# Kernel optimization log

Hardware: AMD Instinct MI355X
Metric: run time of the kernel (lower is better)

The kernel has to match this reference:

```python
import jax, jax.numpy as jnp
import numpy as np

B, L, D, H = 2, 8192, 1024, 16
HD = D // H  # head_dim = 64


def setup_inputs() -> dict:
    key = jax.random.key(0)
    ks = jax.random.split(key, 5)
    s = 1.0 / np.sqrt(D)
    return {
        "x": jax.random.normal(ks[0], (B, L, D), dtype=jnp.float32),
        "Wq": jax.random.normal(ks[1], (D, D), dtype=jnp.float32) * s,
        "bq": jnp.zeros((D,), dtype=jnp.float32),
        "Wk": jax.random.normal(ks[2], (D, D), dtype=jnp.float32) * s,
        "bk": jnp.zeros((D,), dtype=jnp.float32),
        "Wv": jax.random.normal(ks[3], (D, D), dtype=jnp.float32) * s,
        "bv": jnp.zeros((D,), dtype=jnp.float32),
        "Wo": jax.random.normal(ks[4], (D, D), dtype=jnp.float32) * s,
        "bo": jnp.zeros((D,), dtype=jnp.float32),
    }


def _rotary(seq_len, dim):
    pos = jnp.arange(seq_len, dtype=jnp.float32)
    freq = 1.0 / (10000.0 ** (jnp.arange(0, dim, 2, dtype=jnp.float32) / dim))
    ang = pos[:, None] * freq[None, :]               # (L, dim/2)
    sin, cos = jnp.sin(ang), jnp.cos(ang)
    # interleave-duplicate: stack((s,s),-1).reshape(L,dim)  (matches torch code)
    sin = jnp.stack((sin, sin), axis=-1).reshape(seq_len, dim)
    cos = jnp.stack((cos, cos), axis=-1).reshape(seq_len, dim)
    return sin, cos


def _rotate_half(t):
    t1, t2 = jnp.split(t, 2, axis=-1)
    return jnp.concatenate([-t2, t1], axis=-1)


def reference(x, Wq, bq, Wk, bk, Wv, bv, Wo, bo):
    b, l, d = x.shape
    q = (x @ Wq + bq).reshape(b, l, H, HD)
    k = (x @ Wk + bk).reshape(b, l, H, HD)
    v = (x @ Wv + bv).reshape(b, l, H, HD)

    sin, cos = _rotary(l, HD)
    sin = sin[None, :, None, :]  # (1, L, 1, HD)
    cos = cos[None, :, None, :]
    q = q * cos + _rotate_half(q) * sin
    k = k * cos + _rotate_half(k) * sin

    # NOTE: faithful to original — heads NOT transposed to (B,H,L,HD),
    # so scores are (B, L, H, H): attention mixes across heads per position.
    scores = jnp.einsum('blhd,bled->blhe', q, k) / jnp.sqrt(jnp.float32(HD))
    w = jax.nn.softmax(scores, axis=-1)              # dropout = identity (eval)
    out = jnp.einsum('blhe,bled->blhd', w, v).reshape(b, l, d)
    return out @ Wo + bo
```

## Files before the change

kernel.cpp:

```cpp
#include <hip/hip_runtime.h>
#include <hip/hip_bf16.h>

typedef __bf16 bf16_t;
typedef __bf16 bf16x8 __attribute__((ext_vector_type(8)));
typedef float f32x4 __attribute__((ext_vector_type(4)));

#define SEQ_L 8192
#define DMODEL 1024
#define NHEAD 16
#define HDIM 64
static constexpr int MROWS = 2 * SEQ_L;

__device__ __forceinline__ void async_cp16(const bf16_t* g, bf16_t* l) {
  __builtin_amdgcn_global_load_lds(
      (__attribute__((address_space(1))) void*)(void*)(g),
      (__attribute__((address_space(3))) void*)(void*)(l), 16, 0, 0);
}
__device__ __forceinline__ void wg_barrier() { __builtin_amdgcn_s_barrier(); }

__global__ __launch_bounds__(256) void f32_to_bf16_k(const float* __restrict__ in,
                                                     bf16_t* __restrict__ out, int n) {
  int i = (blockIdx.x * 256 + threadIdx.x) * 8;
  if (i >= n) return;
  float4 a = *(const float4*)(in + i);
  float4 b = *(const float4*)(in + i + 4);
  bf16x8 o;
  o[0] = (__bf16)a.x; o[1] = (__bf16)a.y; o[2] = (__bf16)a.z; o[3] = (__bf16)a.w;
  o[4] = (__bf16)b.x; o[5] = (__bf16)b.y; o[6] = (__bf16)b.z; o[7] = (__bf16)b.w;
  *(bf16x8*)(out + i) = o;
}

__global__ __launch_bounds__(256) void w_to_bt_k(
    const float* __restrict__ W0, const float* __restrict__ W1,
    const float* __restrict__ W2, const float* __restrict__ W3,
    bf16_t* __restrict__ T0, bf16_t* __restrict__ T1,
    bf16_t* __restrict__ T2, bf16_t* __restrict__ T3) {
  __shared__ float tile[32][33];
  const int z = blockIdx.z;
  const float* W = (z == 0) ? W0 : (z == 1) ? W1 : (z == 2) ? W2 : W3;
  bf16_t* T = (z == 0) ? T0 : (z == 1) ? T1 : (z == 2) ? T2 : T3;
  const int bx = blockIdx.x, by = blockIdx.y;
  const int tx = threadIdx.x, ty = threadIdx.y;
#pragma unroll
  for (int r = 0; r < 4; ++r)
    tile[ty + r * 8][tx] = W[(size_t)(by * 32 + ty + r * 8) * DMODEL + bx * 32 + tx];
  __syncthreads();
#pragma unroll
  for (int r = 0; r < 4; ++r)
    T[(size_t)(bx * 32 + ty + r * 8) * DMODEL + by * 32 + tx] = (bf16_t)tile[tx][ty + r * 8];
}

__global__ __launch_bounds__(256) void rope_tab_k(float2* __restrict__ tab) {
  int i = blockIdx.x * 256 + threadIdx.x;
  int pos = i >> 5, j = i & 31;
  double freq = pow(10000.0, -(double)j / 32.0);
  double ang = (double)pos * freq;
  tab[i] = make_float2((float)cos(ang), (float)sin(ang));
}

template <int MODE>
__global__ __launch_bounds__(256, 4) void gemm128(
    const bf16_t* __restrict__ A, const bf16_t* __restrict__ Bt,
    const float* __restrict__ b0, const float* __restrict__ b1,
    const float* __restrict__ b2, const float2* __restrict__ rope,
    void* __restrict__ O0, void* __restrict__ O1, void* __restrict__ O2) {
  constexpr int K = DMODEL;
  constexpr int NS = K / 32;
  __shared__ bf16_t As_[2][128 * 32];
  __shared__ bf16_t Bs_[2][128 * 32];
  const int tid = threadIdx.x;
  const int lane = tid & 63;
  const int wave = tid >> 6;
  const int wm = wave >> 1;
  const int wn = wave & 1;
  const size_t row0 = (size_t)blockIdx.x * 128;
  const int col0 = blockIdx.y * 128;
  const int fr = lane & 15;
  const int fke = (lane >> 4) * 8;

  const bf16_t* gA = A + (row0 + (tid >> 2)) * K + (tid & 3) * 8;
  const bf16_t* gB = Bt + ((size_t)col0 + (tid >> 2)) * K + (tid & 3) * 8;

#define STAGE(j, buf)                                      \
  do {                                                     \
    async_cp16(gA + (j)*32, &As_[buf][tid * 8]);           \
    async_cp16(gA + 64 * K + (j)*32, &As_[buf][2048 + tid * 8]); \
    async_cp16(gB + (j)*32, &Bs_[buf][tid * 8]);           \
    async_cp16(gB + 64 * K + (j)*32, &Bs_[buf][2048 + tid * 8]); \
  } while (0)
#define RD(base, row) (*(const bf16x8*)((base) + (row)*32 + fke))
#define VMCNT(n) asm volatile("s_waitcnt vmcnt(" #n ")")
#define SCHED_FENCE() __builtin_amdgcn_sched_barrier(0)

  f32x4 acc[4][4] = {};
  bf16x8 a4[4], b4[4];

#define KSTEP(CUR, DO_STAGE, JNEXT)                                            \
  do {                                                                         \
    if (DO_STAGE) STAGE(JNEXT, (CUR) ^ 1);                                     \
    _Pragma("unroll") for (int f = 0; f < 4; ++f)                              \
        a4[f] = RD(As_[CUR], wm * 64 + f * 16 + fr);                           \
    _Pragma("unroll") for (int n = 0; n < 4; ++n)                              \
        b4[n] = RD(Bs_[CUR], wn * 64 + n * 16 + fr);                           \
    __builtin_amdgcn_s_setprio(1);                                             \
    _Pragma("unroll") for (int f = 0; f < 4; ++f)                              \
        _Pragma("unroll") for (int n = 0; n < 4; ++n)                          \
            acc[f][n] = __builtin_amdgcn_mfma_f32_16x16x32_bf16(               \
                a4[f], b4[n], acc[f][n], 0, 0, 0);                             \
    __builtin_amdgcn_s_setprio(0);                                             \
    VMCNT(0);                                                                  \
    wg_barrier();                                                              \
    SCHED_FENCE();                                                             \
  } while (0)

  STAGE(0, 0);
  VMCNT(0);
  wg_barrier();
  SCHED_FENCE();

#pragma unroll 1
  for (int mm = 0; mm < NS / 2; ++mm) {
    const int m0 = 2 * mm;
    KSTEP(0, true, m0 + 1);
    KSTEP(1, (mm < NS / 2 - 1), m0 + 2);
  }
#undef KSTEP
#undef STAGE
#undef RD
#undef VMCNT
#undef SCHED_FENCE

  const int lr = (lane >> 4) * 4;
  const int lc = lane & 15;
  const int gcol = col0 + wn * 64;
  int which = 0;
  const float* bias = b0;
  int ocol = gcol;
  if constexpr (MODE == 0) {
    which = gcol >> 10;
    bias = (which == 0) ? b0 : (which == 1) ? b1 : b2;
    ocol = gcol - (which << 10);
  }
  const bool do_rope = (MODE == 0) && (which < 2);
  bf16_t* Cb = nullptr;
  float* Cf = nullptr;
  if constexpr (MODE == 0)
    Cb = (bf16_t*)((which == 0) ? O0 : (which == 1) ? O1 : O2);
  else
    Cf = (float*)O0;

#pragma unroll
  for (int mf = 0; mf < 4; ++mf) {
#pragma unroll
    for (int i = 0; i < 4; ++i) {
      const size_t grow = row0 + wm * 64 + mf * 16 + lr + i;
      float vv[4];
#pragma unroll
      for (int n = 0; n < 4; ++n) vv[n] = acc[mf][n][i] + bias[ocol + n * 16 + lc];
      if (do_rope) {
        const int pos = (int)(grow & (size_t)(SEQ_L - 1));
        const float2* rp = rope + (size_t)pos * 32 + (lc >> 1);
        float rv[4];
#pragma unroll
        for (int n = 0; n < 4; ++n) {
          float2 cs = rp[n * 8];
          rv[n] = (n < 2) ? vv[n] * cs.x - vv[n + 2] * cs.y
                          : vv[n] * cs.x + vv[n - 2] * cs.y;
        }
#pragma unroll
        for (int n = 0; n < 4; ++n) vv[n] = rv[n];
      }
      const size_t cbase = grow * (size_t)DMODEL + ocol + lc;
      if constexpr (MODE == 1) {
#pragma unroll
        for (int n = 0; n < 4; ++n) Cf[cbase + n * 16] = vv[n];
      } else {
#pragma unroll
        for (int n = 0; n < 4; ++n) Cb[cbase + n * 16] = (bf16_t)vv[n];
      }
    }
  }
}

__global__ __launch_bounds__(256) void attn_heads_k(const bf16_t* __restrict__ qb,
                                                    const bf16_t* __restrict__ kb,
                                                    const bf16_t* __restrict__ vb,
                                                    bf16_t* __restrict__ ob) {
  const int t = blockIdx.x * 256 + threadIdx.x;
  const int row = t >> 4;
  const int h = t & 15;
  const size_t rbase = (size_t)row * DMODEL;

  float q[HDIM];
#pragma unroll
  for (int j = 0; j < 8; ++j) {
    bf16x8 v8 = *(const bf16x8*)(qb + rbase + h * HDIM + j * 8);
#pragma unroll
    for (int u = 0; u < 8; ++u) q[j * 8 + u] = (float)v8[u];
  }
  float s[NHEAD];
#pragma unroll
  for (int e = 0; e < NHEAD; ++e) {
    float a = 0.f;
#pragma unroll
    for (int j = 0; j < 8; ++j) {
      bf16x8 k8 = *(const bf16x8*)(kb + rbase + e * HDIM + j * 8);
#pragma unroll
      for (int u = 0; u < 8; ++u) a += q[j * 8 + u] * (float)k8[u];
    }
    s[e] = a * 0.125f;
  }
  float mx = s[0];
#pragma unroll
  for (int e = 1; e < NHEAD; ++e) mx = fmaxf(mx, s[e]);
  float sum = 0.f;
#pragma unroll
  for (int e = 0; e < NHEAD; ++e) {
    s[e] = __expf(s[e] - mx);
    sum += s[e];
  }
  const float inv = 1.f / sum;
  float o[HDIM] = {};
#pragma unroll
  for (int e = 0; e < NHEAD; ++e) {
    const float w = s[e] * inv;
#pragma unroll
    for (int j = 0; j < 8; ++j) {
      bf16x8 v8 = *(const bf16x8*)(vb + rbase + e * HDIM + j * 8);
#pragma unroll
      for (int u = 0; u < 8; ++u) o[j * 8 + u] += w * (float)v8[u];
    }
  }
#pragma unroll
  for (int j = 0; j < 8; ++j) {
    bf16x8 st;
#pragma unroll
    for (int u = 0; u < 8; ++u) st[u] = (__bf16)o[j * 8 + u];
    *(bf16x8*)(ob + rbase + h * HDIM + j * 8) = st;
  }
}

extern "C" void kernel_launch(void* const* d_in, const int* in_sizes, int n_in,
                              void* d_out, int out_size, void* d_ws, size_t ws_size,
                              hipStream_t stream) {
  const float* x = (const float*)d_in[0];
  const float* Wq = (const float*)d_in[1];
  const float* bq = (const float*)d_in[2];
  const float* Wk = (const float*)d_in[3];
  const float* bk = (const float*)d_in[4];
  const float* Wv = (const float*)d_in[5];
  const float* bv = (const float*)d_in[6];
  const float* Wo = (const float*)d_in[7];
  const float* bo = (const float*)d_in[8];

  const int M = MROWS, N = DMODEL, K = DMODEL;

  char* p = (char*)d_ws;
  bf16_t* xb = (bf16_t*)p;    p += (size_t)M * K * 2;
  bf16_t* Wqkvt = (bf16_t*)p; p += (size_t)3 * N * K * 2;
  bf16_t* Wot = (bf16_t*)p;   p += (size_t)N * K * 2;
  bf16_t* qb = (bf16_t*)p;    p += (size_t)M * N * 2;
  bf16_t* kb = (bf16_t*)p;    p += (size_t)M * N * 2;
  bf16_t* vb = (bf16_t*)p;    p += (size_t)M * N * 2;
  bf16_t* ab = (bf16_t*)p;    p += (size_t)M * N * 2;
  float2* rope = (float2*)p;  p += (size_t)SEQ_L * 32 * sizeof(float2);

  bf16_t* Wqt = Wqkvt;
  bf16_t* Wkt = Wqkvt + (size_t)N * K;
  bf16_t* Wvt = Wqkvt + (size_t)2 * N * K;

  f32_to_bf16_k<<<(M * K) / (256 * 8), 256, 0, stream>>>(x, xb, M * K);
  w_to_bt_k<<<dim3(32, 32, 4), dim3(32, 8), 0, stream>>>(Wq, Wk, Wv, Wo, Wqt, Wkt, Wvt, Wot);
  rope_tab_k<<<(SEQ_L * 32) / 256, 256, 0, stream>>>(rope);

  gemm128<0><<<dim3(M / 128, (3 * N) / 128), 256, 0, stream>>>(
      xb, Wqkvt, bq, bk, bv, rope, (void*)qb, (void*)kb, (void*)vb);
  attn_heads_k<<<(M * NHEAD) / 256, 256, 0, stream>>>(qb, kb, vb, ab);
  gemm128<1><<<dim3(M / 128, N / 128), 256, 0, stream>>>(
      ab, Wot, bo, nullptr, nullptr, nullptr, d_out, nullptr, nullptr);
}
```

Baseline: 249.6 us.

## Deepen GEMM K-tile to 64 with XOR-swizzled LDS layout

Doubles the K depth of each staged tile from 32 to 64, which halves the number of barrier/wait iterations in the main loop and issues twice as many async global-to-LDS copies per stage. The LDS layout is XOR-swizzled by row so that the 16-byte MFMA fragment reads avoid bank conflicts across the 128-byte rows. The cost is doubled LDS use per block (64 KB total), which may limit how many blocks fit per CU under the launch bound of 4.

```diff
diff --git a/kernel.cpp b/kernel.cpp
--- a/kernel.cpp
+++ b/kernel.cpp
@@ -11,7 +11,7 @@
 #define HDIM 64
 static constexpr int MROWS = 2 * SEQ_L;
 
-__device__ __forceinline__ void async_cp16(const bf16_t* g, bf16_t* l) {
+__device__ __forceinline__ void async_cp16(const void* g, bf16_t* l) {
   __builtin_amdgcn_global_load_lds(
       (__attribute__((address_space(1))) void*)(void*)(g),
       (__attribute__((address_space(3))) void*)(void*)(l), 16, 0, 0);
@@ -65,9 +65,9 @@
     const float* __restrict__ b2, const float2* __restrict__ rope,
     void* __restrict__ O0, void* __restrict__ O1, void* __restrict__ O2) {
   constexpr int K = DMODEL;
-  constexpr int NS = K / 32;
-  __shared__ bf16_t As_[2][128 * 32];
-  __shared__ bf16_t Bs_[2][128 * 32];
+  constexpr int KT = K / 64;
+  __shared__ bf16_t As_[2][128 * 64];
+  __shared__ bf16_t Bs_[2][128 * 64];
   const int tid = threadIdx.x;
   const int lane = tid & 63;
   const int wave = tid >> 6;
@@ -76,40 +76,52 @@
   const size_t row0 = (size_t)blockIdx.x * 128;
   const int col0 = blockIdx.y * 128;
   const int fr = lane & 15;
-  const int fke = (lane >> 4) * 8;
-
-  const bf16_t* gA = A + (row0 + (tid >> 2)) * K + (tid & 3) * 8;
-  const bf16_t* gB = Bt + ((size_t)col0 + (tid >> 2)) * K + (tid & 3) * 8;
-
-#define STAGE(j, buf)                                      \
-  do {                                                     \
-    async_cp16(gA + (j)*32, &As_[buf][tid * 8]);           \
-    async_cp16(gA + 64 * K + (j)*32, &As_[buf][2048 + tid * 8]); \
-    async_cp16(gB + (j)*32, &Bs_[buf][tid * 8]);           \
-    async_cp16(gB + 64 * K + (j)*32, &Bs_[buf][2048 + tid * 8]); \
-  } while (0)
-#define RD(base, row) (*(const bf16x8*)((base) + (row)*32 + fke))
+  const int g4 = lane >> 4;
+
+  const int srow = lane >> 3;
+  const int sch = (lane & 7) ^ srow;
+  const bf16_t* gA = A + (row0 + wave * 32 + srow) * K + sch * 8;
+  const bf16_t* gB = Bt + ((size_t)col0 + wave * 32 + srow) * K + sch * 8;
+
 #define VMCNT(n) asm volatile("s_waitcnt vmcnt(" #n ")")
 #define SCHED_FENCE() __builtin_amdgcn_sched_barrier(0)
+#define STAGE(j, buf)                                                     \
+  do {                                                                    \
+    bf16_t* lA = &As_[buf][wave * 2048 + lane * 8];                       \
+    bf16_t* lB = &Bs_[buf][wave * 2048 + lane * 8];                       \
+    async_cp16(gA + (j)*64, lA);                                          \
+    async_cp16(gA + 8 * K + (j)*64, lA + 512);                            \
+    async_cp16(gA + 16 * K + (j)*64, lA + 1024);                          \
+    async_cp16(gA + 24 * K + (j)*64, lA + 1536);                          \
+    async_cp16(gB + (j)*64, lB);                                          \
+    async_cp16(gB + 8 * K + (j)*64, lB + 512);                            \
+    async_cp16(gB + 16 * K + (j)*64, lB + 1024);                          \
+    async_cp16(gB + 24 * K + (j)*64, lB + 1536);                          \
+  } while (0)
+#define RD(base, row, h)                                                  \
+  (*(const bf16x8*)((const char*)(base) + (size_t)(row)*128 +             \
+                    ((((h)*4 + g4) ^ ((row)&7)) << 4)))
 
   f32x4 acc[4][4] = {};
   bf16x8 a4[4], b4[4];
 
 #define KSTEP(CUR, DO_STAGE, JNEXT)                                            \
   do {                                                                         \
-    if (DO_STAGE) STAGE(JNEXT, (CUR) ^ 1);                                     \
-    _Pragma("unroll") for (int f = 0; f < 4; ++f)                              \
-        a4[f] = RD(As_[CUR], wm * 64 + f * 16 + fr);                           \
-    _Pragma("unroll") for (int n = 0; n < 4; ++n)                              \
-        b4[n] = RD(Bs_[CUR], wn * 64 + n * 16 + fr);                           \
-    __builtin_amdgcn_s_setprio(1);                                             \
-    _Pragma("unroll") for (int f = 0; f < 4; ++f)                              \
-        _Pragma("unroll") for (int n = 0; n < 4; ++n)                          \
-            acc[f][n] = __builtin_amdgcn_mfma_f32_16x16x32_bf16(               \
-                a4[f], b4[n], acc[f][n], 0, 0, 0);                             \
-    __builtin_amdgcn_s_setprio(0);                                             \
-    VMCNT(0);                                                                  \
-    wg_barrier();                                                              \
+    if (DO_STAGE) STAGE(JNEXT, (CUR) ^ 1);   \
+    _Pragma("unroll") for (int h = 0; h < 2; ++h) {                            \
+      _Pragma("unroll") for (int f = 0; f < 4; ++f)                            \
+          a4[f] = RD(As_[CUR], wm * 64 + f * 16 + fr, h);                      \
+      _Pragma("unroll") for (int n = 0; n < 4; ++n)                            \
+          b4[n] = RD(Bs_[CUR], wn * 64 + n * 16 + fr, h);                      \
+      __builtin_amdgcn_s_setprio(1);                                           \
+      _Pragma("unroll") for (int f = 0; f < 4; ++f)                            \
+          _Pragma("unroll") for (int n = 0; n < 4; ++n)                        \
+              acc[f][n] = __builtin_amdgcn_mfma_f32_16x16x32_bf16(             \
+                  a4[f], b4[n], acc[f][n], 0, 0, 0);                           \
+      __builtin_amdgcn_s_setprio(0);                                           \
+    }                                                                          \
+    VMCNT(0);        \
+    wg_barrier();        \
     SCHED_FENCE();                                                             \
   } while (0)
 
@@ -119,10 +131,9 @@
   SCHED_FENCE();
 
 #pragma unroll 1
-  for (int mm = 0; mm < NS / 2; ++mm) {
-    const int m0 = 2 * mm;
-    KSTEP(0, true, m0 + 1);
-    KSTEP(1, (mm < NS / 2 - 1), m0 + 2);
+  for (int mm = 0; mm < KT / 2; ++mm) {
+    KSTEP(0, true, 2 * mm + 1);
+    KSTEP(1, (mm < KT / 2 - 1), 2 * mm + 2);
   }
 #undef KSTEP
 #undef STAGE
@@ -130,7 +141,7 @@
 #undef VMCNT
 #undef SCHED_FENCE
 
-  const int lr = (lane >> 4) * 4;
+  const int lr = g4 * 4;
   const int lc = lane & 15;
   const int gcol = col0 + wn * 64;
   int which = 0;
```

Measured after the change: 261.0 us. +4.5%, slower.
